# Optimization experiments

Hardware: AMD Instinct MI355X
Metric: run time of the kernel (lower is better)

## Reference

```python
import jax, jax.numpy as jnp
import numpy as np

B, H, W, C = 4, 64, 64, 256
CQ = C // 8


def setup_inputs() -> dict:
    key = jax.random.key(0)
    ks = jax.random.split(key, 5)
    scale = 0.02
    inputs = jax.random.normal(ks[0], (B, H, W, C), dtype=jnp.float32)
    wq = jax.random.normal(ks[1], (C, CQ), dtype=jnp.float32) * scale
    bq = jnp.zeros((CQ,), dtype=jnp.float32)
    wk = jax.random.normal(ks[2], (C, CQ), dtype=jnp.float32) * scale
    bk = jnp.zeros((CQ,), dtype=jnp.float32)
    wv = jax.random.normal(ks[3], (C, C), dtype=jnp.float32) * scale
    bv = jnp.zeros((C,), dtype=jnp.float32)
    gamma = jax.random.normal(ks[4], (), dtype=jnp.float32)
    return {"inputs": inputs, "wq": wq, "bq": bq, "wk": wk, "bk": bk,
            "wv": wv, "bv": bv, "gamma": gamma}


def reference(inputs, wq, bq, wk, bk, wv, bv, gamma):
    b, h, w, c = inputs.shape
    n = h * w
    x = inputs.reshape(b, n, c)  # [B, N, C]
    # 1x1 convs == per-pixel linear projections
    q = x @ wq + bq              # [B, N, Cq]
    k = x @ wk + bk              # [B, N, Cq]
    v = x @ wv + bv              # [B, N, C]
    # energy = Q K^T (no sqrt scaling, as in the original)
    energy = jnp.einsum('bnd,bmd->bnm', q, k)      # [B, N, N]
    attention = jax.nn.softmax(energy, axis=-1)    # softmax over keys
    # x_out = V^T @ attention^T -> per query: sum_m attn[n,m] * v[m]
    x_out = jnp.einsum('bnm,bmc->bnc', attention, v)  # [B, N, C]
    x_out = x_out.reshape(b, h, w, c)
    return gamma * x_out + inputs
```

## Files before the change

### kernel.cpp

```cpp
#include <hip/hip_runtime.h>
#include <hip/hip_bf16.h>

typedef __attribute__((ext_vector_type(8))) short bf16x8;
typedef __attribute__((ext_vector_type(4))) float f32x4;
typedef __attribute__((ext_vector_type(4))) int int4v;

#define NB 4
#define NN 4096
#define NC 256
#define NSPLIT 4
#define KEYS_PER_SPLIT 1024
#define KT_ITERS 16

__device__ __forceinline__ unsigned short f2bf(float f) {
    unsigned u = __builtin_bit_cast(unsigned, f);
    u += 0x7fffu + ((u >> 16) & 1u);
    return (unsigned short)(u >> 16);
}
__device__ __forceinline__ float bf2f(unsigned short u) {
    unsigned v = ((unsigned)u) << 16;
    return __builtin_bit_cast(float, v);
}
__device__ __forceinline__ void load_lds16(const void* g, void* l) {
    __builtin_amdgcn_global_load_lds(
        (const __attribute__((address_space(1))) void*)g,
        (__attribute__((address_space(3))) void*)l, 16, 0, 0);
}

__global__ __launch_bounds__(256) void wt_kernel(
    const float* __restrict__ wq, const float* __restrict__ wk,
    const float* __restrict__ wv, unsigned short* __restrict__ wt)
{
    const int c = blockIdx.x;
    const int k = threadIdx.x;
    float v;
    if (c < 32)      v = wq[k * 32 + c];
    else if (c < 64) v = wk[k * 32 + (c - 32)];
    else             v = wv[k * 256 + (c - 64)];
    wt[c * 256 + k] = f2bf(v);
}

__global__ __launch_bounds__(256) void proj_kernel(
    const float* __restrict__ x,
    const unsigned short* __restrict__ wt,
    const float* __restrict__ bq, const float* __restrict__ bk,
    const float* __restrict__ bv,
    unsigned short* __restrict__ q_ws,
    unsigned short* __restrict__ k_ws,
    unsigned short* __restrict__ vt_ws)
{
    const int lane = threadIdx.x & 63;
    const int w    = threadIdx.x >> 6;
    const int l15  = lane & 15, hh = lane >> 4;
    const int m0   = blockIdx.x * 16;
    const int ct0  = w * 5;

    f32x4 acc[5];
    #pragma unroll
    for (int i = 0; i < 5; ++i) acc[i] = f32x4{0.f, 0.f, 0.f, 0.f};

    const float* xrow = x + (size_t)(m0 + l15) * 256 + hh * 8;
    #pragma unroll
    for (int ks = 0; ks < 8; ++ks) {
        float4 xa = ((const float4*)(xrow + ks * 32))[0];
        float4 xb = ((const float4*)(xrow + ks * 32))[1];
        bf16x8 afrag;
        afrag[0] = (short)f2bf(xa.x); afrag[1] = (short)f2bf(xa.y);
        afrag[2] = (short)f2bf(xa.z); afrag[3] = (short)f2bf(xa.w);
        afrag[4] = (short)f2bf(xb.x); afrag[5] = (short)f2bf(xb.y);
        afrag[6] = (short)f2bf(xb.z); afrag[7] = (short)f2bf(xb.w);
        #pragma unroll
        for (int c = 0; c < 5; ++c) {
            bf16x8 bfrag = *(const bf16x8*)(wt + (size_t)((ct0 + c) * 16 + l15) * 256 + ks * 32 + hh * 8);
            acc[c] = __builtin_amdgcn_mfma_f32_16x16x32_bf16(afrag, bfrag, acc[c], 0, 0, 0);
        }
    }

    const int b    = m0 >> 12;
    const int nloc = m0 & 4095;
    #pragma unroll
    for (int c = 0; c < 5; ++c) {
        const int ct = ct0 + c;
        const int c0 = ct * 16;
        float bias;
        if (c0 < 32)      bias = bq[c0 + l15];
        else if (c0 < 64) bias = bk[c0 - 32 + l15];
        else              bias = bv[c0 - 64 + l15];
        if (c0 < 64) {
            unsigned short* dst = (c0 < 32) ? q_ws : k_ws;
            const int cc = (c0 < 32) ? c0 : (c0 - 32);
            #pragma unroll
            for (int i = 0; i < 4; ++i)
                dst[(size_t)(m0 + hh * 4 + i) * 32 + cc + l15] = f2bf(acc[c][i] + bias);
        } else {
            const int cc = c0 - 64 + l15;
            #pragma unroll
            for (int i = 0; i < 4; i += 2) {
                unsigned lo = f2bf(acc[c][i]     + bias);
                unsigned hi = f2bf(acc[c][i + 1] + bias);
                *(unsigned*)(vt_ws + ((size_t)b * 256 + cc) * 4096 + nloc + hh * 4 + i)
                    = lo | (hi << 16);
            }
        }
    }
}

__global__ __launch_bounds__(256, 3) void attn_kernel(
    const unsigned short* __restrict__ q_ws,
    const unsigned short* __restrict__ k_ws,
    const unsigned short* __restrict__ vt_ws,
    unsigned short* __restrict__ opart,
    float* __restrict__ lpart)
{
    __shared__ unsigned short vt_lds[256 * 64];
    __shared__ unsigned short p_lds[64 * 64];
    __shared__ float l_red[2][64];

    const int lane = threadIdx.x & 63;
    const int wid  = threadIdx.x >> 6;
    const int l15  = lane & 15, hh = lane >> 4;
    const int split = blockIdx.x >> 8;
    const int rem   = blockIdx.x & 255;
    const int b     = rem >> 6;
    const int q0    = (rem & 63) * 64;
    const int wq    = wid >> 1;
    const int wc    = wid & 1;
    const int key0  = split * KEYS_PER_SPLIT;

    bf16x8 aq[2];
    #pragma unroll
    for (int qt = 0; qt < 2; ++qt)
        aq[qt] = *(const bf16x8*)(q_ws + (size_t)(b * 4096 + q0 + wq * 32 + qt * 16 + l15) * 32 + hh * 8);

    f32x4 acc[2][8];
    float lsum[2][4];
    #pragma unroll
    for (int qt = 0; qt < 2; ++qt) {
        #pragma unroll
        for (int ct = 0; ct < 8; ++ct) acc[qt][ct] = f32x4{0.f, 0.f, 0.f, 0.f};
        #pragma unroll
        for (int i = 0; i < 4; ++i) lsum[qt][i] = 0.f;
    }

    const unsigned short* vt_base = vt_ws + (size_t)b * 256 * 4096;
    const unsigned short* k_base  = k_ws + (size_t)b * 4096 * 32;

    for (int kt = 0; kt < KT_ITERS; ++kt) {
        const int kb = key0 + kt * 64;
        __syncthreads();

        #pragma unroll
        for (int e = 0; e < 8; ++e) {
            int idx  = e * 256 + threadIdx.x;
            int c    = idx >> 3;
            int slot = idx & 7;
            const unsigned short* src = vt_base + (size_t)c * 4096 + kb + ((slot ^ (c & 7)) << 3);
            load_lds16(src, (char*)vt_lds + idx * 16);
        }

        bf16x8 bkf[2];
        #pragma unroll
        for (int g = 0; g < 2; ++g)
            bkf[g] = *(const bf16x8*)(k_base + (size_t)(kb + wc * 32 + g * 16 + l15) * 32 + hh * 8);
        f32x4 e2[2][2];
        #pragma unroll
        for (int qt = 0; qt < 2; ++qt) {
            #pragma unroll
            for (int g = 0; g < 2; ++g) {
                f32x4 z = {0.f, 0.f, 0.f, 0.f};
                e2[qt][g] = __builtin_amdgcn_mfma_f32_16x16x32_bf16(aq[qt], bkf[g], z, 0, 0, 0);
            }
        }

        #pragma unroll
        for (int qt = 0; qt < 2; ++qt) {
            #pragma unroll
            for (int g = 0; g < 2; ++g) {
                #pragma unroll
                for (int i = 0; i < 4; ++i) {
                    float p = __expf(e2[qt][g][i]);
                    lsum[qt][i] += p;
                    int r   = wq * 32 + qt * 16 + hh * 4 + i;
                    int off = (wc * 32 + g * 16 + l15) * 2;
                    int sw  = (((off >> 4) ^ (r & 7)) << 4) | (off & 15);
                    *(unsigned short*)((char*)p_lds + r * 128 + sw) = f2bf(p);
                }
            }
        }
        __syncthreads();

        #pragma unroll
        for (int s = 0; s < 2; ++s) {
            bf16x8 ap[2];
            #pragma unroll
            for (int qt = 0; qt < 2; ++qt) {
                int r = wq * 32 + qt * 16 + l15;
                ap[qt] = *(const bf16x8*)((char*)p_lds + r * 128 + (((s * 4 + hh) ^ (r & 7)) << 4));
            }
            #pragma unroll
            for (int ct = 0; ct < 8; ++ct) {
                int c = wc * 128 + ct * 16 + l15;
                bf16x8 bvf = *(const bf16x8*)((char*)vt_lds + c * 128 + (((s * 4 + hh) ^ (c & 7)) << 4));
                #pragma unroll
                for (int qt = 0; qt < 2; ++qt)
                    acc[qt][ct] = __builtin_amdgcn_mfma_f32_16x16x32_bf16(ap[qt], bvf, acc[qt][ct], 0, 0, 0);
            }
        }
    }

    __syncthreads();
    #pragma unroll
    for (int qt = 0; qt < 2; ++qt) {
        #pragma unroll
        for (int i = 0; i < 4; ++i) {
            float s = lsum[qt][i];
            s += __shfl_xor(s, 1); s += __shfl_xor(s, 2);
            s += __shfl_xor(s, 4); s += __shfl_xor(s, 8);
            if (l15 == 0) l_red[wc][wq * 32 + qt * 16 + hh * 4 + i] = s;
        }
    }
    __syncthreads();

    const size_t rowbase = (size_t)(split * 4 + b) * 4096 + q0;
    #pragma unroll
    for (int qt = 0; qt < 2; ++qt) {
        #pragma unroll
        for (int i = 0; i < 4; ++i) {
            int r = wq * 32 + qt * 16 + hh * 4 + i;
            if (wc == 0 && l15 == 0) {
                float lt = l_red[0][r] + l_red[1][r];
                lpart[rowbase + r] = lt;
            }
            #pragma unroll
            for (int ct = 0; ct < 8; ++ct) {
                int c = wc * 128 + ct * 16 + l15;
                opart[(rowbase + r) * 256 + c] = f2bf(acc[qt][ct][i]);
            }
        }
    }
}

__global__ __launch_bounds__(256) void combine_kernel(
    const unsigned short* __restrict__ opart,
    const float* __restrict__ lpart,
    const float* __restrict__ x,
    const float* __restrict__ gamma_p,
    float* __restrict__ out)
{
    const int t  = blockIdx.x * 256 + threadIdx.x;
    const int r  = t >> 5;
    const int c0 = (t & 31) * 8;
    const float gamma = gamma_p[0];

    float sumO[8];
    #pragma unroll
    for (int j = 0; j < 8; ++j) sumO[j] = 0.f;
    float suml = 0.f;
    #pragma unroll
    for (int s = 0; s < NSPLIT; ++s) {
        bf16x8 o = *(const bf16x8*)(opart + ((size_t)(s * 16384 + r)) * 256 + c0);
        #pragma unroll
        for (int j = 0; j < 8; ++j) sumO[j] += bf2f((unsigned short)o[j]);
        suml += lpart[s * 16384 + r];
    }
    const float inv = gamma / suml;
    const size_t base = (size_t)r * 256 + c0;
    float4 x0 = *(const float4*)(x + base);
    float4 x1 = *(const float4*)(x + base + 4);
    float4 o0, o1;
    o0.x = sumO[0] * inv + x0.x; o0.y = sumO[1] * inv + x0.y;
    o0.z = sumO[2] * inv + x0.z; o0.w = sumO[3] * inv + x0.w;
    o1.x = sumO[4] * inv + x1.x; o1.y = sumO[5] * inv + x1.y;
    o1.z = sumO[6] * inv + x1.z; o1.w = sumO[7] * inv + x1.w;
    *(float4*)(out + base)     = o0;
    *(float4*)(out + base + 4) = o1;
}

extern "C" void kernel_launch(void* const* d_in, const int* in_sizes, int n_in,
                              void* d_out, int out_size, void* d_ws, size_t ws_size,
                              hipStream_t stream) {
    const float* x     = (const float*)d_in[0];
    const float* wq    = (const float*)d_in[1];
    const float* bq    = (const float*)d_in[2];
    const float* wk    = (const float*)d_in[3];
    const float* bk    = (const float*)d_in[4];
    const float* wv    = (const float*)d_in[5];
    const float* bv    = (const float*)d_in[6];
    const float* gamma = (const float*)d_in[7];
    float* out = (float*)d_out;

    char* ws = (char*)d_ws;
    unsigned short* wt    = (unsigned short*)(ws);
    unsigned short* q_ws  = (unsigned short*)(ws + 163840);
    unsigned short* k_ws  = (unsigned short*)(ws + 1212416);
    unsigned short* vt_ws = (unsigned short*)(ws + 2260992);
    unsigned short* opart = (unsigned short*)(ws + 10649600);
    float*          lpart = (float*)(ws + 44204032);

    wt_kernel     <<<320,  256, 0, stream>>>(wq, wk, wv, wt);
    proj_kernel   <<<1024, 256, 0, stream>>>(x, wt, bq, bk, bv, q_ws, k_ws, vt_ws);
    attn_kernel   <<<1024, 256, 0, stream>>>(q_ws, k_ws, vt_ws, opart, lpart);
    combine_kernel<<<2048, 256, 0, stream>>>(opart, lpart, x, gamma, out);
}
```

Baseline: 114.0 us.

## Enlarge attention tile to 128 queries with 8 waves and XCD-aware block mapping

The attention kernel now runs 512-thread blocks covering 128 queries each, halving the grid. Each loaded V^T tile of 64 keys is therefore reused across twice as many queries, which cuts global-to-LDS traffic per unit of work. Blocks are also remapped so each XCD handles a fixed (split, batch) pair, aiming for better L2 locality, and s_setprio is raised around the PV MFMA section. Each wave holds a 4x4 accumulator tile, and LDS use grows, both of which may reduce occupancy.

```diff
diff --git a/kernel.cpp b/kernel.cpp
--- a/kernel.cpp
+++ b/kernel.cpp
@@ -105,7 +105,7 @@
     }
 }
 
-__global__ __launch_bounds__(256, 3) void attn_kernel(
+__global__ __launch_bounds__(512, 4) void attn_kernel(
     const unsigned short* __restrict__ q_ws,
     const unsigned short* __restrict__ k_ws,
     const unsigned short* __restrict__ vt_ws,
@@ -113,31 +113,35 @@
     float* __restrict__ lpart)
 {
     __shared__ unsigned short vt_lds[256 * 64];
-    __shared__ unsigned short p_lds[64 * 64];
-    __shared__ float l_red[2][64];
+    __shared__ unsigned short p_lds[128 * 64];
 
     const int lane = threadIdx.x & 63;
     const int wid  = threadIdx.x >> 6;
     const int l15  = lane & 15, hh = lane >> 4;
-    const int split = blockIdx.x >> 8;
-    const int rem   = blockIdx.x & 255;
-    const int b     = rem >> 6;
-    const int q0    = (rem & 63) * 64;
-    const int wq    = wid >> 1;
-    const int wc    = wid & 1;
+
+    const int xcd   = blockIdx.x & 7;
+    const int j     = blockIdx.x >> 3;
+    const int combo = xcd * 2 + (j >> 5);
+    const int qtile = j & 31;
+    const int split = combo >> 2;
+    const int b     = combo & 3;
+    const int q0    = qtile * 128;
     const int key0  = split * KEYS_PER_SPLIT;
 
-    bf16x8 aq[2];
-    #pragma unroll
-    for (int qt = 0; qt < 2; ++qt)
-        aq[qt] = *(const bf16x8*)(q_ws + (size_t)(b * 4096 + q0 + wq * 32 + qt * 16 + l15) * 32 + hh * 8);
-
-    f32x4 acc[2][8];
-    float lsum[2][4];
-    #pragma unroll
-    for (int qt = 0; qt < 2; ++qt) {
-        #pragma unroll
-        for (int ct = 0; ct < 8; ++ct) acc[qt][ct] = f32x4{0.f, 0.f, 0.f, 0.f};
+    const int wr   = wid >> 2;
+    const int kc   = wid & 3;
+
+    bf16x8 aq[4];
+    #pragma unroll
+    for (int qt = 0; qt < 4; ++qt)
+        aq[qt] = *(const bf16x8*)(q_ws + (size_t)(b * 4096 + q0 + wr * 64 + qt * 16 + l15) * 32 + hh * 8);
+
+    f32x4 acc[4][4];
+    float lsum[4][4];
+    #pragma unroll
+    for (int qt = 0; qt < 4; ++qt) {
+        #pragma unroll
+        for (int ct = 0; ct < 4; ++ct) acc[qt][ct] = f32x4{0.f, 0.f, 0.f, 0.f};
         #pragma unroll
         for (int i = 0; i < 4; ++i) lsum[qt][i] = 0.f;
     }
@@ -150,90 +154,92 @@
         __syncthreads();
 
         #pragma unroll
-        for (int e = 0; e < 8; ++e) {
-            int idx  = e * 256 + threadIdx.x;
+        for (int e = 0; e < 4; ++e) {
+            int idx  = e * 512 + threadIdx.x;
             int c    = idx >> 3;
             int slot = idx & 7;
             const unsigned short* src = vt_base + (size_t)c * 4096 + kb + ((slot ^ (c & 7)) << 3);
             load_lds16(src, (char*)vt_lds + idx * 16);
         }
 
-        bf16x8 bkf[2];
-        #pragma unroll
-        for (int g = 0; g < 2; ++g)
-            bkf[g] = *(const bf16x8*)(k_base + (size_t)(kb + wc * 32 + g * 16 + l15) * 32 + hh * 8);
-        f32x4 e2[2][2];
-        #pragma unroll
-        for (int qt = 0; qt < 2; ++qt) {
-            #pragma unroll
-            for (int g = 0; g < 2; ++g) {
-                f32x4 z = {0.f, 0.f, 0.f, 0.f};
-                e2[qt][g] = __builtin_amdgcn_mfma_f32_16x16x32_bf16(aq[qt], bkf[g], z, 0, 0, 0);
-            }
-        }
-
-        #pragma unroll
-        for (int qt = 0; qt < 2; ++qt) {
-            #pragma unroll
-            for (int g = 0; g < 2; ++g) {
-                #pragma unroll
-                for (int i = 0; i < 4; ++i) {
-                    float p = __expf(e2[qt][g][i]);
-                    lsum[qt][i] += p;
-                    int r   = wq * 32 + qt * 16 + hh * 4 + i;
-                    int off = (wc * 32 + g * 16 + l15) * 2;
-                    int sw  = (((off >> 4) ^ (r & 7)) << 4) | (off & 15);
-                    *(unsigned short*)((char*)p_lds + r * 128 + sw) = f2bf(p);
-                }
+        bf16x8 bkf = *(const bf16x8*)(k_base + (size_t)(kb + kc * 16 + l15) * 32 + hh * 8);
+        f32x4 e2[4];
+        #pragma unroll
+        for (int qt = 0; qt < 4; ++qt) {
+            f32x4 z = {0.f, 0.f, 0.f, 0.f};
+            e2[qt] = __builtin_amdgcn_mfma_f32_16x16x32_bf16(aq[qt], bkf, z, 0, 0, 0);
+        }
+
+        #pragma unroll
+        for (int qt = 0; qt < 4; ++qt) {
+            #pragma unroll
+            for (int i = 0; i < 4; ++i) {
+                float p = __expf(e2[qt][i]);
+                lsum[qt][i] += p;
+                int r   = wr * 64 + qt * 16 + hh * 4 + i;
+                int off = kc * 32 + l15 * 2;
+                int sw  = (((off >> 4) ^ (r & 7)) << 4) | (off & 15);
+                *(unsigned short*)((char*)p_lds + r * 128 + sw) = f2bf(p);
             }
         }
         __syncthreads();
 
+        __builtin_amdgcn_s_setprio(1);
         #pragma unroll
         for (int s = 0; s < 2; ++s) {
-            bf16x8 ap[2];
-            #pragma unroll
-            for (int qt = 0; qt < 2; ++qt) {
-                int r = wq * 32 + qt * 16 + l15;
+            bf16x8 ap[4];
+            #pragma unroll
+            for (int qt = 0; qt < 4; ++qt) {
+                int r = wr * 64 + qt * 16 + l15;
                 ap[qt] = *(const bf16x8*)((char*)p_lds + r * 128 + (((s * 4 + hh) ^ (r & 7)) << 4));
             }
             #pragma unroll
-            for (int ct = 0; ct < 8; ++ct) {
-                int c = wc * 128 + ct * 16 + l15;
+            for (int ct = 0; ct < 4; ++ct) {
+                int c = kc * 64 + ct * 16 + l15;
                 bf16x8 bvf = *(const bf16x8*)((char*)vt_lds + c * 128 + (((s * 4 + hh) ^ (c & 7)) << 4));
                 #pragma unroll
-                for (int qt = 0; qt < 2; ++qt)
+                for (int qt = 0; qt < 4; ++qt)
                     acc[qt][ct] = __builtin_amdgcn_mfma_f32_16x16x32_bf16(ap[qt], bvf, acc[qt][ct], 0, 0, 0);
             }
         }
+        __builtin_amdgcn_s_setprio(0);
     }
 
     __syncthreads();
-    #pragma unroll
-    for (int qt = 0; qt < 2; ++qt) {
+    float* l_s = (float*)p_lds;
+    #pragma unroll
+    for (int qt = 0; qt < 4; ++qt) {
         #pragma unroll
         for (int i = 0; i < 4; ++i) {
             float s = lsum[qt][i];
             s += __shfl_xor(s, 1); s += __shfl_xor(s, 2);
             s += __shfl_xor(s, 4); s += __shfl_xor(s, 8);
-            if (l15 == 0) l_red[wc][wq * 32 + qt * 16 + hh * 4 + i] = s;
+            if (l15 == 0) l_s[kc * 128 + wr * 64 + qt * 16 + hh * 4 + i] = s;
         }
     }
     __syncthreads();
 
-    const size_t rowbase = (size_t)(split * 4 + b) * 4096 + q0;
-    #pragma unroll
-    for (int qt = 0; qt < 2; ++qt) {
+    const size_t rowbase = (size_t)(split * 4 + b) * 4096 + q0 + wr * 64;
+    if (kc == 0 && l15 == 0) {
+        #pragma unroll
+        for (int qt = 0; qt < 4; ++qt) {
+            #pragma unroll
+            for (int i = 0; i < 4; ++i) {
+                int row = wr * 64 + qt * 16 + hh * 4 + i;
+                lpart[rowbase + qt * 16 + hh * 4 + i] =
+                    l_s[row] + l_s[128 + row] + l_s[256 + row] + l_s[384 + row];
+            }
+        }
+    }
+
+    #pragma unroll
+    for (int qt = 0; qt < 4; ++qt) {
         #pragma unroll
         for (int i = 0; i < 4; ++i) {
-            int r = wq * 32 + qt * 16 + hh * 4 + i;
-            if (wc == 0 && l15 == 0) {
-                float lt = l_red[0][r] + l_red[1][r];
-                lpart[rowbase + r] = lt;
-            }
-            #pragma unroll
-            for (int ct = 0; ct < 8; ++ct) {
-                int c = wc * 128 + ct * 16 + l15;
+            int r = qt * 16 + hh * 4 + i;
+            #pragma unroll
+            for (int ct = 0; ct < 4; ++ct) {
+                int c = kc * 64 + ct * 16 + l15;
                 opart[(rowbase + r) * 256 + c] = f2bf(acc[qt][ct][i]);
             }
         }
@@ -299,6 +305,6 @@
 
     wt_kernel     <<<320,  256, 0, stream>>>(wq, wk, wv, wt);
     proj_kernel   <<<1024, 256, 0, stream>>>(x, wt, bq, bk, bv, q_ws, k_ws, vt_ws);
-    attn_kernel   <<<1024, 256, 0, stream>>>(q_ws, k_ws, vt_ws, opart, lpart);
+    attn_kernel   <<<512,  512, 0, stream>>>(q_ws, k_ws, vt_ws, opart, lpart);
     combine_kernel<<<2048, 256, 0, stream>>>(opart, lpart, x, gamma, out);
 }
```

Result: slower. 121.0 us (+6.1%).
